# Kernel optimization log

Measured on AMD Instinct MI355X. Metric: run time of the kernel, lower is better.

## Reference

```python
import jax, jax.numpy as jnp
import numpy as np

C = 256
EPS = 1e-5


def dwconv3x3(x, w):
    # x: [B,C,H,W], w: [C,1,3,3] depthwise (groups=C)
    return jax.lax.conv_general_dilated(
        x, w, window_strides=(1, 1), padding=((1, 1), (1, 1)),
        dimension_numbers=('NCHW', 'OIHW', 'NCHW'), feature_group_count=x.shape[1])


def bn(x, gamma, beta, mean, var):
    # inference-mode batchnorm over channel dim of NCHW
    inv = gamma * jax.lax.rsqrt(var + EPS)
    return x * inv[:, None, None] + (beta - mean * inv)[:, None, None]


def setup_inputs() -> dict:
    key = jax.random.key(0)
    ks = jax.random.split(key, 8)
    B, H, W = 32, 64, 64
    inp = {
        'x': jax.random.normal(ks[0], (B, C, H, W), jnp.float32),
        'edge_w': jax.random.normal(ks[1], (C, 1, 3, 3), jnp.float32) * 0.1,
        'edge_gamma': jnp.ones((C,), jnp.float32),
        'edge_beta': jnp.zeros((C,), jnp.float32),
        'edge_mean': jnp.zeros((C,), jnp.float32),
        'edge_var': jnp.ones((C,), jnp.float32),
        'fc1_w': jax.random.normal(ks[2], (C // 16, C), jnp.float32) * 0.05,
        'fc2_w': jax.random.normal(ks[3], (C, C // 16), jnp.float32) * 0.05,
        'fusion_w': jax.random.normal(ks[4], (C, 2 * C), jnp.float32) * 0.05,
        'fusion_b': jnp.zeros((C,), jnp.float32),
        'bn1_gamma': jnp.ones((C,), jnp.float32),
        'bn1_beta': jnp.zeros((C,), jnp.float32),
        'bn1_mean': jnp.zeros((C,), jnp.float32),
        'bn1_var': jnp.ones((C,), jnp.float32),
        'deform_w': jax.random.normal(ks[5], (C, 1, 3, 3), jnp.float32) * 0.1,
        'balance_w': jax.random.normal(ks[6], (C, C), jnp.float32) * 0.05,
        'balance_b': jnp.zeros((C,), jnp.float32),
        'bn2_gamma': jnp.ones((C,), jnp.float32),
        'bn2_beta': jnp.zeros((C,), jnp.float32),
        'bn2_mean': jnp.zeros((C,), jnp.float32),
        'bn2_var': jnp.ones((C,), jnp.float32),
    }
    return inp


def reference(x, edge_w, edge_gamma, edge_beta, edge_mean, edge_var,
              fc1_w, fc2_w, fusion_w, fusion_b,
              bn1_gamma, bn1_beta, bn1_mean, bn1_var,
              deform_w, balance_w, balance_b,
              bn2_gamma, bn2_beta, bn2_mean, bn2_var):
    # --- EdgeEnhancementAttention ---
    edge = jax.nn.relu(bn(dwconv3x3(x, edge_w), edge_gamma, edge_beta, edge_mean, edge_var))
    # SE channel attention
    avg = jnp.mean(x, axis=(2, 3))                       # [B,C]
    att = jax.nn.relu(avg @ fc1_w.T)                     # [B,C/16]
    att = jax.nn.sigmoid(att @ fc2_w.T)                  # [B,C]
    enhanced = x * att[:, :, None, None]
    fused = jnp.concatenate([enhanced, edge], axis=1)    # [B,2C,H,W]
    out = jnp.einsum('bchw,oc->bohw', fused, fusion_w) + fusion_b[None, :, None, None]
    out = bn(out, bn1_gamma, bn1_beta, bn1_mean, bn1_var)
    # --- DeformConv2d with zero offsets == plain depthwise 3x3 conv, no bias ---
    out = dwconv3x3(out, deform_w)
    # --- balance: 1x1 conv + BN, then gate by input ---
    out = jnp.einsum('bchw,oc->bohw', out, balance_w) + balance_b[None, :, None, None]
    out = bn(out, bn2_gamma, bn2_beta, bn2_mean, bn2_var)
    return out * x
```

## Files before the change

kernel.cpp:

```cpp
#include <hip/hip_runtime.h>
#include <math.h>

#define HW 4096
#define PLSTRIDE ((size_t)HW * 8)

typedef unsigned short ushort_t;
typedef short v8s __attribute__((ext_vector_type(8)));
typedef float v4f __attribute__((ext_vector_type(4)));

__device__ __forceinline__ float bf2f(ushort_t u) {
    union { unsigned int i; float f; } v; v.i = ((unsigned int)u) << 16; return v.f;
}
__device__ __forceinline__ ushort_t f2bf(float f) {
    unsigned int x = __float_as_uint(f);
    x += 0x7fffu + ((x >> 16) & 1u);
    return (ushort_t)(x >> 16);
}

__device__ __forceinline__ void gld16(const ushort_t* g, ushort_t* l) {
    __builtin_amdgcn_global_load_lds(
        (__attribute__((address_space(1))) void*)g,
        (__attribute__((address_space(3))) void*)l, 16, 0, 0);
}

__global__ __launch_bounds__(256) void k_consts(
    const float* eg, const float* ebt, const float* em, const float* ev,
    const float* fb,
    const float* g1, const float* b1, const float* m1, const float* v1,
    const float* balb,
    const float* g2, const float* b2, const float* m2, const float* v2,
    float* cbuf)
{
    int c = threadIdx.x;
    float iE = eg[c] * rsqrtf(ev[c] + 1e-5f);
    cbuf[c]       = iE;
    cbuf[256 + c] = ebt[c] - em[c] * iE;
    float i1 = g1[c] * rsqrtf(v1[c] + 1e-5f);
    cbuf[512 + c] = i1;
    cbuf[768 + c] = b1[c] - m1[c] * i1 + fb[c] * i1;
    float i2 = g2[c] * rsqrtf(v2[c] + 1e-5f);
    cbuf[1024 + c] = i2;
    cbuf[1280 + c] = b2[c] - m2[c] * i2 + balb[c] * i2;
}

__global__ __launch_bounds__(256) void k_wcopy(const float* fusw, const float* balw,
                                               ushort_t* fusw2b, ushort_t* balwb)
{
    int o = blockIdx.x, t = threadIdx.x;
    fusw2b[o * 256 + t] = f2bf(fusw[o * 512 + 256 + t]);
    balwb[o * 256 + t]  = f2bf(balw[o * 256 + t]);
}

__global__ __launch_bounds__(512) void k_edge(const float* x, const float* ew,
                                              const float* cbuf, ushort_t* A,
                                              float* avg)
{
    __shared__ __align__(16) ushort_t Xs[4096];
    __shared__ __align__(16) ushort_t Es[4096];
    int cg = blockIdx.x;
    int b = blockIdx.y;
    int t = threadIdx.x;
    int w = t & 63;
    int pl = t >> 6;
    int c = cg * 8 + pl;
    const float* px = x + ((size_t)(b * 256 + c)) * HW;
    ushort_t* AX = A + ((size_t)(b * 64 + cg)) * PLSTRIDE;
    ushort_t* AE = A + ((size_t)(b * 64 + 32 + cg)) * PLSTRIDE;
    float wt[9];
    #pragma unroll
    for (int k = 0; k < 9; ++k) wt[k] = ew[c * 9 + k];
    float sE = cbuf[c], cE = cbuf[256 + c];
    bool wl = (w > 0), wrr = (w < 63);

    float p0l = 0.f, p0c = 0.f, p0r = 0.f;
    float p1l, p1c, p1r;
    p1c = px[w];
    p1l = wl ? px[w - 1] : 0.f;
    p1r = wrr ? px[w + 1] : 0.f;
    float s = 0.f;
    for (int hb = 0; hb < 8; ++hb) {
        #pragma unroll
        for (int hi = 0; hi < 8; ++hi) {
            int h = hb * 8 + hi;
            float p2l, p2c, p2r;
            if (h < 63) {
                const float* row = px + (h + 1) * 64;
                p2c = row[w];
                p2l = wl ? row[w - 1] : 0.f;
                p2r = wrr ? row[w + 1] : 0.f;
            } else {
                p2l = p2c = p2r = 0.f;
            }
            float a = p0l * wt[0] + p0c * wt[1] + p0r * wt[2]
                    + p1l * wt[3] + p1c * wt[4] + p1r * wt[5]
                    + p2l * wt[6] + p2c * wt[7] + p2r * wt[8];
            s += p1c;
            float v = a * sE + cE;
            Es[hi * 512 + w * 8 + pl] = f2bf(v > 0.f ? v : 0.f);
            Xs[hi * 512 + w * 8 + pl] = f2bf(p1c);
            p0l = p1l; p0c = p1c; p0r = p1r;
            p1l = p2l; p1c = p2c; p1r = p2r;
        }
        __syncthreads();
        {
            int hwg = (hb * 8 + pl) * 64 + w;
            uint4 vx = *(const uint4*)&Xs[pl * 512 + w * 8];
            uint4 ve = *(const uint4*)&Es[pl * 512 + w * 8];
            *(uint4*)(AX + (size_t)hwg * 8) = vx;
            *(uint4*)(AE + (size_t)hwg * 8) = ve;
        }
        __syncthreads();
    }
    #pragma unroll
    for (int off = 32; off > 0; off >>= 1) s += __shfl_down(s, off, 64);
    if ((t & 63) == 0) avg[b * 256 + c] = s * (1.0f / HW);
}

__global__ __launch_bounds__(256) void k_sefold(const float* avg, const float* fc1,
                                                const float* fc2, const float* fusw,
                                                ushort_t* w1b)
{
    int b = blockIdx.x, t = threadIdx.x;
    __shared__ float av[256];
    __shared__ float hid[16];
    av[t] = avg[b * 256 + t];
    __syncthreads();
    if (t < 16) {
        float h = 0.f;
        for (int c = 0; c < 256; ++c) h += av[c] * fc1[t * 256 + c];
        hid[t] = h > 0.f ? h : 0.f;
    }
    __syncthreads();
    float a = 0.f;
    #pragma unroll
    for (int j = 0; j < 16; ++j) a += hid[j] * fc2[t * 16 + j];
    float att = 1.0f / (1.0f + expf(-a));
    ushort_t* wout = w1b + (size_t)b * 65536;
    for (int o = 0; o < 256; ++o)
        wout[o * 256 + t] = f2bf(fusw[o * 512 + t] * att);
}

__global__ __launch_bounds__(512) void k_gemm1(ushort_t* __restrict__ A,
                                               const ushort_t* __restrict__ w1b,
                                               const ushort_t* __restrict__ fusw2b,
                                               const float* __restrict__ cbuf)
{
    __shared__ __align__(16) ushort_t At[8][64 * 64];
    int hw0 = blockIdx.x * 64;
    int b = blockIdx.y;
    int t = threadIdx.x;
    int lane = t & 63, wv = t >> 6;
    int quad = lane >> 4, l16 = lane & 15;
    int wr = wv >> 2, wc = wv & 3;

    int mrow0 = wv * 8 + (lane >> 3);
    int cswz = (lane & 7) ^ (mrow0 & 7);
    const ushort_t* srcK = A + ((size_t)(b * 64 + cswz)) * PLSTRIDE
                             + ((size_t)(hw0 + mrow0)) * 8;
    #pragma unroll
    for (int kb = 0; kb < 8; ++kb)
        gld16(srcK + (size_t)(kb * 8) * PLSTRIDE, &At[kb][wv * 8 * 64]);

    v4f acc[2][4];
    #pragma unroll
    for (int i = 0; i < 2; ++i)
        #pragma unroll
        for (int j = 0; j < 4; ++j) acc[i][j] = (v4f){0.f, 0.f, 0.f, 0.f};

    const ushort_t* rowA[4];
    const ushort_t* rowB[4];
    int oo[4];
    #pragma unroll
    for (int nt = 0; nt < 4; ++nt) {
        int o = wc * 64 + nt * 16 + l16;
        oo[nt] = o;
        rowA[nt] = w1b + ((size_t)(b * 256 + o)) * 256;
        rowB[nt] = fusw2b + (size_t)o * 256;
    }

#define LDB1(dst, kbv) { \
    _Pragma("unroll") for (int ks2 = 0; ks2 < 2; ++ks2) { \
        int kg = (kbv) * 64 + ks2 * 32 + quad * 8; \
        _Pragma("unroll") for (int nt = 0; nt < 4; ++nt) { \
            dst[ks2][nt] = ((kbv) < 4) ? *(const v8s*)(rowA[nt] + kg) \
                                       : *(const v8s*)(rowB[nt] + (kg - 256)); \
        } } }

#define COMP1(kbv, bsrc) { \
    _Pragma("unroll") for (int ks2 = 0; ks2 < 2; ++ks2) { \
        v8s afr[2]; \
        _Pragma("unroll") for (int mt = 0; mt < 2; ++mt) { \
            int ml = wr * 32 + mt * 16 + l16; \
            int jj = (ks2 * 4 + quad) ^ (ml & 7); \
            afr[mt] = *(const v8s*)(&At[kbv][ml * 64 + jj * 8]); \
        } \
        _Pragma("unroll") for (int mt = 0; mt < 2; ++mt) \
            _Pragma("unroll") for (int nt = 0; nt < 4; ++nt) \
                acc[mt][nt] = __builtin_amdgcn_mfma_f32_16x16x32_bf16( \
                    afr[mt], bsrc[ks2][nt], acc[mt][nt], 0, 0, 0); \
    } }

    v8s bq0[2][4], bq1[2][4];
    LDB1(bq0, 0);
    __syncthreads();
    #pragma unroll 1
    for (int kb = 0; kb < 8; kb += 2) {
        LDB1(bq1, kb + 1);
        COMP1(kb, bq0);
        if (kb < 6) LDB1(bq0, kb + 2);
        COMP1(kb + 1, bq1);
    }
#undef LDB1
#undef COMP1

    #pragma unroll
    for (int nt = 0; nt < 4; ++nt) {
        int o = oo[nt];
        float s1 = cbuf[512 + o], c1 = cbuf[768 + o];
        ushort_t* op = A + ((size_t)(b * 64 + 32 + (o >> 3))) * PLSTRIDE + (o & 7);
        #pragma unroll
        for (int mt = 0; mt < 2; ++mt)
            #pragma unroll
            for (int r = 0; r < 4; ++r) {
                int m = hw0 + wr * 32 + mt * 16 + quad * 4 + r;
                op[(size_t)m * 8] = f2bf(acc[mt][nt][r] * s1 + c1);
            }
    }
}

__global__ __launch_bounds__(256) void k_dw2(ushort_t* A, const float* dfw)
{
    int h = blockIdx.x;
    int b = blockIdx.y;
    int t = threadIdx.x;
    int wc = t & 7;
    int cg = t >> 3;
    int c0 = cg * 8;
    int w0 = wc * 8;

    float acc[8][8];
    #pragma unroll
    for (int w = 0; w < 8; ++w)
        #pragma unroll
        for (int ch = 0; ch < 8; ++ch) acc[w][ch] = 0.f;

    const ushort_t* pE = A + ((size_t)(b * 64 + 32 + cg)) * PLSTRIDE;
    #pragma unroll
    for (int r = 0; r < 3; ++r) {
        int hh = h - 1 + r;
        if (hh < 0 || hh > 63) continue;
        float wtr[3][8];
        #pragma unroll
        for (int d = 0; d < 3; ++d)
            #pragma unroll
            for (int ch = 0; ch < 8; ++ch)
                wtr[d][ch] = dfw[(c0 + ch) * 9 + r * 3 + d];
        const ushort_t* row = pE + (size_t)(hh * 64) * 8;
        uint4 rv[10];
        #pragma unroll
        for (int j = 0; j < 10; ++j) {
            int col = w0 - 1 + j;
            if (col >= 0 && col < 64)
                rv[j] = *(const uint4*)(row + (size_t)col * 8);
            else
                rv[j] = (uint4){0u, 0u, 0u, 0u};
        }
        #pragma unroll
        for (int j = 0; j < 10; ++j) {
            unsigned int wd[4] = { rv[j].x, rv[j].y, rv[j].z, rv[j].w };
            float v[8];
            #pragma unroll
            for (int i = 0; i < 8; ++i)
                v[i] = bf2f((i & 1) ? (ushort_t)(wd[i >> 1] >> 16)
                                    : (ushort_t)(wd[i >> 1] & 0xffff));
            if (j <= 7)
                #pragma unroll
                for (int ch = 0; ch < 8; ++ch) acc[j][ch] += v[ch] * wtr[0][ch];
            if (j >= 1 && j <= 8)
                #pragma unroll
                for (int ch = 0; ch < 8; ++ch) acc[j - 1][ch] += v[ch] * wtr[1][ch];
            if (j >= 2)
                #pragma unroll
                for (int ch = 0; ch < 8; ++ch) acc[j - 2][ch] += v[ch] * wtr[2][ch];
        }
    }
    ushort_t* pX = A + ((size_t)(b * 64 + cg)) * PLSTRIDE + (size_t)(h * 64 + w0) * 8;
    #pragma unroll
    for (int w = 0; w < 8; ++w) {
        uint4 ov;
        ov.x = (unsigned int)f2bf(acc[w][0]) | ((unsigned int)f2bf(acc[w][1]) << 16);
        ov.y = (unsigned int)f2bf(acc[w][2]) | ((unsigned int)f2bf(acc[w][3]) << 16);
        ov.z = (unsigned int)f2bf(acc[w][4]) | ((unsigned int)f2bf(acc[w][5]) << 16);
        ov.w = (unsigned int)f2bf(acc[w][6]) | ((unsigned int)f2bf(acc[w][7]) << 16);
        *(uint4*)(pX + (size_t)w * 8) = ov;
    }
}

__global__ __launch_bounds__(512) void k_gemm2(ushort_t* __restrict__ A,
                                               const ushort_t* __restrict__ balwb)
{
    __shared__ __align__(16) ushort_t At[4][128 * 64];
    int hw0 = blockIdx.x * 128;
    int b = blockIdx.y;
    int t = threadIdx.x;
    int lane = t & 63, wv = t >> 6;
    int quad = lane >> 4, l16 = lane & 15;
    int wr = wv >> 2, wc = wv & 3;

    int mrow0 = wv * 16 + (lane >> 3);
    int cswz = (lane & 7) ^ (mrow0 & 7);
    const ushort_t* srcK = A + ((size_t)(b * 64 + cswz)) * PLSTRIDE
                             + ((size_t)(hw0 + mrow0)) * 8;
    #pragma unroll
    for (int kb = 0; kb < 4; ++kb) {
        const ushort_t* sp = srcK + (size_t)(kb * 8) * PLSTRIDE;
        gld16(sp, &At[kb][(wv * 16) * 64]);
        gld16(sp + 64, &At[kb][(wv * 16 + 8) * 64]);
    }

    v4f acc[4][4];
    #pragma unroll
    for (int i = 0; i < 4; ++i)
        #pragma unroll
        for (int j = 0; j < 4; ++j) acc[i][j] = (v4f){0.f, 0.f, 0.f, 0.f};

    const ushort_t* rowW[4];
    int oo[4];
    #pragma unroll
    for (int nt = 0; nt < 4; ++nt) {
        int o = wc * 64 + nt * 16 + l16;
        oo[nt] = o;
        rowW[nt] = balwb + (size_t)o * 256;
    }

#define LDB2(dst, kbv) { \
    _Pragma("unroll") for (int ks2 = 0; ks2 < 2; ++ks2) { \
        int kg = (kbv) * 64 + ks2 * 32 + quad * 8; \
        _Pragma("unroll") for (int nt = 0; nt < 4; ++nt) \
            dst[ks2][nt] = *(const v8s*)(rowW[nt] + kg); \
    } }

#define COMP2(kbv, bsrc) { \
    _Pragma("unroll") for (int ks2 = 0; ks2 < 2; ++ks2) { \
        v8s afr[4]; \
        _Pragma("unroll") for (int mt = 0; mt < 4; ++mt) { \
            int ml = wr * 64 + mt * 16 + l16; \
            int jj = (ks2 * 4 + quad) ^ (ml & 7); \
            afr[mt] = *(const v8s*)(&At[kbv][ml * 64 + jj * 8]); \
        } \
        _Pragma("unroll") for (int mt = 0; mt < 4; ++mt) \
            _Pragma("unroll") for (int nt = 0; nt < 4; ++nt) \
                acc[mt][nt] = __builtin_amdgcn_mfma_f32_16x16x32_bf16( \
                    afr[mt], bsrc[ks2][nt], acc[mt][nt], 0, 0, 0); \
    } }

    v8s bq0[2][4], bq1[2][4];
    LDB2(bq0, 0);
    __syncthreads();
    #pragma unroll 1
    for (int kb = 0; kb < 4; kb += 2) {
        LDB2(bq1, kb + 1);
        COMP2(kb, bq0);
        if (kb < 2) LDB2(bq0, kb + 2);
        COMP2(kb + 1, bq1);
    }
#undef LDB2
#undef COMP2

    #pragma unroll
    for (int nt = 0; nt < 4; ++nt) {
        int o = oo[nt];
        ushort_t* op = A + ((size_t)(b * 64 + 32 + (o >> 3))) * PLSTRIDE + (o & 7);
        #pragma unroll
        for (int mt = 0; mt < 4; ++mt)
            #pragma unroll
            for (int r = 0; r < 4; ++r) {
                int m = hw0 + wr * 64 + mt * 16 + quad * 4 + r;
                op[(size_t)m * 8] = f2bf(acc[mt][nt][r]);
            }
    }
}

__global__ __launch_bounds__(256) void k_final(const ushort_t* A, const float* x,
                                               const float* cbuf, float* out)
{
    __shared__ float Lt[64 * 65];
    int bid = blockIdx.x;
    int b = bid >> 8;
    int rem = bid & 255;
    int hw0 = (rem >> 2) * 64;
    int c0 = (rem & 3) * 64;
    int t = threadIdx.x;
    #pragma unroll
    for (int r = 0; r < 2; ++r) {
        int idx = r * 256 + t;
        int hwl = idx >> 3;
        int cq = idx & 7;
        uint4 v = *(const uint4*)(A + ((size_t)(b * 64 + 32 + (c0 >> 3) + cq)) * PLSTRIDE
                                    + (size_t)(hw0 + hwl) * 8);
        unsigned int wd[4] = { v.x, v.y, v.z, v.w };
        #pragma unroll
        for (int j = 0; j < 8; ++j) {
            ushort_t u = (j & 1) ? (ushort_t)(wd[j >> 1] >> 16) : (ushort_t)(wd[j >> 1] & 0xffff);
            Lt[(cq * 8 + j) * 65 + hwl] = bf2f(u);
        }
    }
    __syncthreads();
    int hw_l = t & 63;
    int c_l0 = t >> 6;
    #pragma unroll
    for (int j = 0; j < 16; ++j) {
        int c_l = c_l0 * 16 + j;
        int c = c0 + c_l;
        float s2 = cbuf[1024 + c], c2 = cbuf[1280 + c];
        size_t g = ((size_t)b * 256 + c) * HW + hw0 + hw_l;
        float xv = x[g];
        out[g] = (Lt[c_l * 65 + hw_l] * s2 + c2) * xv;
    }
}

extern "C" void kernel_launch(void* const* d_in, const int* in_sizes, int n_in,
                              void* d_out, int out_size, void* d_ws, size_t ws_size,
                              hipStream_t stream)
{
    const float* x    = (const float*)d_in[0];
    const float* ew   = (const float*)d_in[1];
    const float* fc1  = (const float*)d_in[6];
    const float* fc2  = (const float*)d_in[7];
    const float* fusw = (const float*)d_in[8];
    const float* dfw  = (const float*)d_in[14];
    const float* balw = (const float*)d_in[15];
    float* out = (float*)d_out;

    char* ws = (char*)d_ws;
    ushort_t* A      = (ushort_t*)(ws);
    ushort_t* w1b    = (ushort_t*)(ws + 134217728);
    ushort_t* fusw2b = (ushort_t*)(ws + 138412032);
    ushort_t* balwb  = (ushort_t*)(ws + 138543104);
    float*    avg    = (float*)(ws + 138674176);
    float*    cbuf   = (float*)(ws + 138706944);

    k_consts<<<1, 256, 0, stream>>>((const float*)d_in[2], (const float*)d_in[3],
                                    (const float*)d_in[4], (const float*)d_in[5],
                                    (const float*)d_in[9],
                                    (const float*)d_in[10], (const float*)d_in[11],
                                    (const float*)d_in[12], (const float*)d_in[13],
                                    (const float*)d_in[16],
                                    (const float*)d_in[17], (const float*)d_in[18],
                                    (const float*)d_in[19], (const float*)d_in[20],
                                    cbuf);
    k_wcopy<<<256, 256, 0, stream>>>(fusw, balw, fusw2b, balwb);
    k_edge<<<dim3(32, 32), 512, 0, stream>>>(x, ew, cbuf, A, avg);
    k_sefold<<<32, 256, 0, stream>>>(avg, fc1, fc2, fusw, w1b);
    k_gemm1<<<dim3(64, 32), 512, 0, stream>>>(A, w1b, fusw2b, cbuf);
    k_dw2<<<dim3(64, 32), 256, 0, stream>>>(A, dfw);
    k_gemm2<<<dim3(32, 32), 512, 0, stream>>>(A, balwb);
    k_final<<<8192, 256, 0, stream>>>(A, x, cbuf, out);
}
```

Baseline: 648.5 us.

## Restructure GEMMs with LDS-staged B tiles, XCD swizzle, and sliding-row depthwise conv

Both 1x1-conv GEMMs now use 128x256 tiles that stage the A and B operands into LDS each K step through global_load_lds, replacing per-lane B register loads. A block-index remap spreads consecutive blocks across XCDs. The depthwise conv is rewritten so each thread owns one column and slides down 32 rows, reusing rows in registers and taking horizontal neighbours via lane shuffles. The final kernel's load indexing is reordered for coalescing. The GEMMs have no double buffering and sync twice per K step, which may expose load latency.

```diff
diff --git a/kernel.cpp b/kernel.cpp
--- a/kernel.cpp
+++ b/kernel.cpp
@@ -140,236 +140,220 @@
         wout[o * 256 + t] = f2bf(fusw[o * 512 + t] * att);
 }
 
-__global__ __launch_bounds__(512) void k_gemm1(ushort_t* __restrict__ A,
-                                               const ushort_t* __restrict__ w1b,
-                                               const ushort_t* __restrict__ fusw2b,
-                                               const float* __restrict__ cbuf)
-{
-    __shared__ __align__(16) ushort_t At[8][64 * 64];
-    int hw0 = blockIdx.x * 64;
-    int b = blockIdx.y;
+__global__ __launch_bounds__(512, 4) void k_gemm1(ushort_t* __restrict__ A,
+                                                  const ushort_t* __restrict__ w1b,
+                                                  const ushort_t* __restrict__ fusw2b,
+                                                  const float* __restrict__ cbuf)
+{
+    __shared__ __align__(16) ushort_t At[128 * 64];
+    __shared__ __align__(16) ushort_t Bt[256 * 64];
+    int bid = blockIdx.x;
+    int orig = (bid & 7) * 128 + (bid >> 3);
+    int b = orig >> 5;
+    int hw0 = (orig & 31) * 128;
     int t = threadIdx.x;
     int lane = t & 63, wv = t >> 6;
     int quad = lane >> 4, l16 = lane & 15;
     int wr = wv >> 2, wc = wv & 3;
-
-    int mrow0 = wv * 8 + (lane >> 3);
-    int cswz = (lane & 7) ^ (mrow0 & 7);
-    const ushort_t* srcK = A + ((size_t)(b * 64 + cswz)) * PLSTRIDE
-                             + ((size_t)(hw0 + mrow0)) * 8;
-    #pragma unroll
-    for (int kb = 0; kb < 8; ++kb)
-        gld16(srcK + (size_t)(kb * 8) * PLSTRIDE, &At[kb][wv * 8 * 64]);
-
-    v4f acc[2][4];
-    #pragma unroll
-    for (int i = 0; i < 2; ++i)
+    int srow = lane >> 3, kch = lane & 7;
+
+    v4f acc[4][4];
+    #pragma unroll
+    for (int i = 0; i < 4; ++i)
         #pragma unroll
         for (int j = 0; j < 4; ++j) acc[i][j] = (v4f){0.f, 0.f, 0.f, 0.f};
 
-    const ushort_t* rowA[4];
-    const ushort_t* rowB[4];
-    int oo[4];
+    for (int kb = 0; kb < 8; ++kb) {
+        __syncthreads();
+        #pragma unroll
+        for (int r = 0; r < 2; ++r) {
+            int mrow = wv * 8 + r * 64 + srow;
+            int csw = kch ^ (mrow & 7);
+            gld16(A + ((size_t)(b * 64 + kb * 8 + csw)) * PLSTRIDE
+                    + (size_t)(hw0 + mrow) * 8,
+                  &At[(wv * 8 + r * 64) * 64]);
+        }
+        #pragma unroll
+        for (int r = 0; r < 4; ++r) {
+            int orow = wv * 8 + r * 64 + srow;
+            int kc2 = kch ^ (orow & 7);
+            const ushort_t* bs = (kb < 4)
+                ? (w1b + ((size_t)(b * 256 + orow)) * 256 + kb * 64 + kc2 * 8)
+                : (fusw2b + ((size_t)orow) * 256 + (kb - 4) * 64 + kc2 * 8);
+            gld16(bs, &Bt[(wv * 8 + r * 64) * 64]);
+        }
+        __syncthreads();
+        #pragma unroll
+        for (int ks2 = 0; ks2 < 2; ++ks2) {
+            v8s afr[4], bfr[4];
+            #pragma unroll
+            for (int mt = 0; mt < 4; ++mt) {
+                int ml = wr * 64 + mt * 16 + l16;
+                int jj = (ks2 * 4 + quad) ^ (ml & 7);
+                afr[mt] = *(const v8s*)(&At[ml * 64 + jj * 8]);
+            }
+            #pragma unroll
+            for (int nt = 0; nt < 4; ++nt) {
+                int ol = wc * 64 + nt * 16 + l16;
+                int jj = (ks2 * 4 + quad) ^ (ol & 7);
+                bfr[nt] = *(const v8s*)(&Bt[ol * 64 + jj * 8]);
+            }
+            #pragma unroll
+            for (int mt = 0; mt < 4; ++mt)
+                #pragma unroll
+                for (int nt = 0; nt < 4; ++nt)
+                    acc[mt][nt] = __builtin_amdgcn_mfma_f32_16x16x32_bf16(
+                        afr[mt], bfr[nt], acc[mt][nt], 0, 0, 0);
+        }
+    }
+
     #pragma unroll
     for (int nt = 0; nt < 4; ++nt) {
         int o = wc * 64 + nt * 16 + l16;
-        oo[nt] = o;
-        rowA[nt] = w1b + ((size_t)(b * 256 + o)) * 256;
-        rowB[nt] = fusw2b + (size_t)o * 256;
-    }
-
-#define LDB1(dst, kbv) { \
-    _Pragma("unroll") for (int ks2 = 0; ks2 < 2; ++ks2) { \
-        int kg = (kbv) * 64 + ks2 * 32 + quad * 8; \
-        _Pragma("unroll") for (int nt = 0; nt < 4; ++nt) { \
-            dst[ks2][nt] = ((kbv) < 4) ? *(const v8s*)(rowA[nt] + kg) \
-                                       : *(const v8s*)(rowB[nt] + (kg - 256)); \
-        } } }
-
-#define COMP1(kbv, bsrc) { \
-    _Pragma("unroll") for (int ks2 = 0; ks2 < 2; ++ks2) { \
-        v8s afr[2]; \
-        _Pragma("unroll") for (int mt = 0; mt < 2; ++mt) { \
-            int ml = wr * 32 + mt * 16 + l16; \
-            int jj = (ks2 * 4 + quad) ^ (ml & 7); \
-            afr[mt] = *(const v8s*)(&At[kbv][ml * 64 + jj * 8]); \
-        } \
-        _Pragma("unroll") for (int mt = 0; mt < 2; ++mt) \
-            _Pragma("unroll") for (int nt = 0; nt < 4; ++nt) \
-                acc[mt][nt] = __builtin_amdgcn_mfma_f32_16x16x32_bf16( \
-                    afr[mt], bsrc[ks2][nt], acc[mt][nt], 0, 0, 0); \
-    } }
-
-    v8s bq0[2][4], bq1[2][4];
-    LDB1(bq0, 0);
-    __syncthreads();
-    #pragma unroll 1
-    for (int kb = 0; kb < 8; kb += 2) {
-        LDB1(bq1, kb + 1);
-        COMP1(kb, bq0);
-        if (kb < 6) LDB1(bq0, kb + 2);
-        COMP1(kb + 1, bq1);
-    }
-#undef LDB1
-#undef COMP1
-
-    #pragma unroll
-    for (int nt = 0; nt < 4; ++nt) {
-        int o = oo[nt];
         float s1 = cbuf[512 + o], c1 = cbuf[768 + o];
         ushort_t* op = A + ((size_t)(b * 64 + 32 + (o >> 3))) * PLSTRIDE + (o & 7);
         #pragma unroll
-        for (int mt = 0; mt < 2; ++mt)
+        for (int mt = 0; mt < 4; ++mt)
             #pragma unroll
             for (int r = 0; r < 4; ++r) {
-                int m = hw0 + wr * 32 + mt * 16 + quad * 4 + r;
+                int m = hw0 + wr * 64 + mt * 16 + quad * 4 + r;
                 op[(size_t)m * 8] = f2bf(acc[mt][nt][r] * s1 + c1);
             }
     }
 }
 
-__global__ __launch_bounds__(256) void k_dw2(ushort_t* A, const float* dfw)
-{
-    int h = blockIdx.x;
+__global__ __launch_bounds__(256) void k_dw2(ushort_t* __restrict__ A,
+                                             const float* __restrict__ dfw)
+{
+    int t = threadIdx.x;
+    int w = t & 63;
+    int pl = t >> 6;
+    int cg = blockIdx.x * 4 + pl;
     int b = blockIdx.y;
-    int t = threadIdx.x;
-    int wc = t & 7;
-    int cg = t >> 3;
-    int c0 = cg * 8;
-    int w0 = wc * 8;
-
-    float acc[8][8];
-    #pragma unroll
-    for (int w = 0; w < 8; ++w)
-        #pragma unroll
-        for (int ch = 0; ch < 8; ++ch) acc[w][ch] = 0.f;
-
+    int h0 = blockIdx.z * 32;
     const ushort_t* pE = A + ((size_t)(b * 64 + 32 + cg)) * PLSTRIDE;
-    #pragma unroll
-    for (int r = 0; r < 3; ++r) {
-        int hh = h - 1 + r;
-        if (hh < 0 || hh > 63) continue;
-        float wtr[3][8];
+    ushort_t* pX = A + ((size_t)(b * 64 + cg)) * PLSTRIDE;
+    float wt[3][3][8];
+    #pragma unroll
+    for (int r = 0; r < 3; ++r)
         #pragma unroll
         for (int d = 0; d < 3; ++d)
             #pragma unroll
             for (int ch = 0; ch < 8; ++ch)
-                wtr[d][ch] = dfw[(c0 + ch) * 9 + r * 3 + d];
-        const ushort_t* row = pE + (size_t)(hh * 64) * 8;
-        uint4 rv[10];
-        #pragma unroll
-        for (int j = 0; j < 10; ++j) {
-            int col = w0 - 1 + j;
-            if (col >= 0 && col < 64)
-                rv[j] = *(const uint4*)(row + (size_t)col * 8);
-            else
-                rv[j] = (uint4){0u, 0u, 0u, 0u};
-        }
-        #pragma unroll
-        for (int j = 0; j < 10; ++j) {
-            unsigned int wd[4] = { rv[j].x, rv[j].y, rv[j].z, rv[j].w };
-            float v[8];
-            #pragma unroll
-            for (int i = 0; i < 8; ++i)
-                v[i] = bf2f((i & 1) ? (ushort_t)(wd[i >> 1] >> 16)
-                                    : (ushort_t)(wd[i >> 1] & 0xffff));
-            if (j <= 7)
-                #pragma unroll
-                for (int ch = 0; ch < 8; ++ch) acc[j][ch] += v[ch] * wtr[0][ch];
-            if (j >= 1 && j <= 8)
-                #pragma unroll
-                for (int ch = 0; ch < 8; ++ch) acc[j - 1][ch] += v[ch] * wtr[1][ch];
-            if (j >= 2)
-                #pragma unroll
-                for (int ch = 0; ch < 8; ++ch) acc[j - 2][ch] += v[ch] * wtr[2][ch];
-        }
-    }
-    ushort_t* pX = A + ((size_t)(b * 64 + cg)) * PLSTRIDE + (size_t)(h * 64 + w0) * 8;
-    #pragma unroll
-    for (int w = 0; w < 8; ++w) {
+                wt[r][d][ch] = dfw[(cg * 8 + ch) * 9 + r * 3 + d];
+    bool wl = (w > 0), wrr = (w < 63);
+
+    uint4 rm, rc, rp;
+    rm = (h0 > 0) ? *(const uint4*)(pE + (size_t)((h0 - 1) * 64 + w) * 8)
+                  : (uint4){0u, 0u, 0u, 0u};
+    rc = *(const uint4*)(pE + (size_t)(h0 * 64 + w) * 8);
+
+#define DWROW(v, r) { \
+    unsigned int cx0 = v.x, cx1 = v.y, cx2 = v.z, cx3 = v.w; \
+    unsigned int lx0 = __shfl_up(cx0, 1, 64), lx1 = __shfl_up(cx1, 1, 64); \
+    unsigned int lx2 = __shfl_up(cx2, 1, 64), lx3 = __shfl_up(cx3, 1, 64); \
+    unsigned int rx0 = __shfl_down(cx0, 1, 64), rx1 = __shfl_down(cx1, 1, 64); \
+    unsigned int rx2 = __shfl_down(cx2, 1, 64), rx3 = __shfl_down(cx3, 1, 64); \
+    unsigned int cw[4] = { cx0, cx1, cx2, cx3 }; \
+    unsigned int lw[4] = { lx0, lx1, lx2, lx3 }; \
+    unsigned int rw[4] = { rx0, rx1, rx2, rx3 }; \
+    _Pragma("unroll") for (int ch = 0; ch < 8; ++ch) { \
+        float fC = bf2f((ch & 1) ? (ushort_t)(cw[ch >> 1] >> 16) \
+                                 : (ushort_t)(cw[ch >> 1] & 0xffff)); \
+        float fL = wl ? bf2f((ch & 1) ? (ushort_t)(lw[ch >> 1] >> 16) \
+                                      : (ushort_t)(lw[ch >> 1] & 0xffff)) : 0.f; \
+        float fR = wrr ? bf2f((ch & 1) ? (ushort_t)(rw[ch >> 1] >> 16) \
+                                       : (ushort_t)(rw[ch >> 1] & 0xffff)) : 0.f; \
+        acc[ch] += fL * wt[r][0][ch] + fC * wt[r][1][ch] + fR * wt[r][2][ch]; \
+    } }
+
+    for (int s = 0; s < 32; ++s) {
+        int h = h0 + s;
+        rp = (h + 1 < 64) ? *(const uint4*)(pE + (size_t)((h + 1) * 64 + w) * 8)
+                          : (uint4){0u, 0u, 0u, 0u};
+        float acc[8];
+        #pragma unroll
+        for (int ch = 0; ch < 8; ++ch) acc[ch] = 0.f;
+        DWROW(rm, 0);
+        DWROW(rc, 1);
+        DWROW(rp, 2);
         uint4 ov;
-        ov.x = (unsigned int)f2bf(acc[w][0]) | ((unsigned int)f2bf(acc[w][1]) << 16);
-        ov.y = (unsigned int)f2bf(acc[w][2]) | ((unsigned int)f2bf(acc[w][3]) << 16);
-        ov.z = (unsigned int)f2bf(acc[w][4]) | ((unsigned int)f2bf(acc[w][5]) << 16);
-        ov.w = (unsigned int)f2bf(acc[w][6]) | ((unsigned int)f2bf(acc[w][7]) << 16);
-        *(uint4*)(pX + (size_t)w * 8) = ov;
-    }
-}
-
-__global__ __launch_bounds__(512) void k_gemm2(ushort_t* __restrict__ A,
-                                               const ushort_t* __restrict__ balwb)
-{
-    __shared__ __align__(16) ushort_t At[4][128 * 64];
-    int hw0 = blockIdx.x * 128;
-    int b = blockIdx.y;
+        ov.x = (unsigned int)f2bf(acc[0]) | ((unsigned int)f2bf(acc[1]) << 16);
+        ov.y = (unsigned int)f2bf(acc[2]) | ((unsigned int)f2bf(acc[3]) << 16);
+        ov.z = (unsigned int)f2bf(acc[4]) | ((unsigned int)f2bf(acc[5]) << 16);
+        ov.w = (unsigned int)f2bf(acc[6]) | ((unsigned int)f2bf(acc[7]) << 16);
+        *(uint4*)(pX + (size_t)(h * 64 + w) * 8) = ov;
+        rm = rc; rc = rp;
+    }
+#undef DWROW
+}
+
+__global__ __launch_bounds__(512, 4) void k_gemm2(ushort_t* __restrict__ A,
+                                                  const ushort_t* __restrict__ balwb)
+{
+    __shared__ __align__(16) ushort_t At[128 * 64];
+    __shared__ __align__(16) ushort_t Bt[256 * 64];
+    int bid = blockIdx.x;
+    int orig = (bid & 7) * 128 + (bid >> 3);
+    int b = orig >> 5;
+    int hw0 = (orig & 31) * 128;
     int t = threadIdx.x;
     int lane = t & 63, wv = t >> 6;
     int quad = lane >> 4, l16 = lane & 15;
     int wr = wv >> 2, wc = wv & 3;
-
-    int mrow0 = wv * 16 + (lane >> 3);
-    int cswz = (lane & 7) ^ (mrow0 & 7);
-    const ushort_t* srcK = A + ((size_t)(b * 64 + cswz)) * PLSTRIDE
-                             + ((size_t)(hw0 + mrow0)) * 8;
-    #pragma unroll
+    int srow = lane >> 3, kch = lane & 7;
+
+    v4f acc[4][4];
+    #pragma unroll
+    for (int i = 0; i < 4; ++i)
+        #pragma unroll
+        for (int j = 0; j < 4; ++j) acc[i][j] = (v4f){0.f, 0.f, 0.f, 0.f};
+
     for (int kb = 0; kb < 4; ++kb) {
-        const ushort_t* sp = srcK + (size_t)(kb * 8) * PLSTRIDE;
-        gld16(sp, &At[kb][(wv * 16) * 64]);
-        gld16(sp + 64, &At[kb][(wv * 16 + 8) * 64]);
-    }
-
-    v4f acc[4][4];
-    #pragma unroll
-    for (int i = 0; i < 4; ++i)
-        #pragma unroll
-        for (int j = 0; j < 4; ++j) acc[i][j] = (v4f){0.f, 0.f, 0.f, 0.f};
-
-    const ushort_t* rowW[4];
-    int oo[4];
+        __syncthreads();
+        #pragma unroll
+        for (int r = 0; r < 2; ++r) {
+            int mrow = wv * 8 + r * 64 + srow;
+            int csw = kch ^ (mrow & 7);
+            gld16(A + ((size_t)(b * 64 + kb * 8 + csw)) * PLSTRIDE
+                    + (size_t)(hw0 + mrow) * 8,
+                  &At[(wv * 8 + r * 64) * 64]);
+        }
+        #pragma unroll
+        for (int r = 0; r < 4; ++r) {
+            int orow = wv * 8 + r * 64 + srow;
+            int kc2 = kch ^ (orow & 7);
+            gld16(balwb + ((size_t)orow) * 256 + kb * 64 + kc2 * 8,
+                  &Bt[(wv * 8 + r * 64) * 64]);
+        }
+        __syncthreads();
+        #pragma unroll
+        for (int ks2 = 0; ks2 < 2; ++ks2) {
+            v8s afr[4], bfr[4];
+            #pragma unroll
+            for (int mt = 0; mt < 4; ++mt) {
+                int ml = wr * 64 + mt * 16 + l16;
+                int jj = (ks2 * 4 + quad) ^ (ml & 7);
+                afr[mt] = *(const v8s*)(&At[ml * 64 + jj * 8]);
+            }
+            #pragma unroll
+            for (int nt = 0; nt < 4; ++nt) {
+                int ol = wc * 64 + nt * 16 + l16;
+                int jj = (ks2 * 4 + quad) ^ (ol & 7);
+                bfr[nt] = *(const v8s*)(&Bt[ol * 64 + jj * 8]);
+            }
+            #pragma unroll
+            for (int mt = 0; mt < 4; ++mt)
+                #pragma unroll
+                for (int nt = 0; nt < 4; ++nt)
+                    acc[mt][nt] = __builtin_amdgcn_mfma_f32_16x16x32_bf16(
+                        afr[mt], bfr[nt], acc[mt][nt], 0, 0, 0);
+        }
+    }
+
     #pragma unroll
     for (int nt = 0; nt < 4; ++nt) {
         int o = wc * 64 + nt * 16 + l16;
-        oo[nt] = o;
-        rowW[nt] = balwb + (size_t)o * 256;
-    }
-
-#define LDB2(dst, kbv) { \
-    _Pragma("unroll") for (int ks2 = 0; ks2 < 2; ++ks2) { \
-        int kg = (kbv) * 64 + ks2 * 32 + quad * 8; \
-        _Pragma("unroll") for (int nt = 0; nt < 4; ++nt) \
-            dst[ks2][nt] = *(const v8s*)(rowW[nt] + kg); \
-    } }
-
-#define COMP2(kbv, bsrc) { \
-    _Pragma("unroll") for (int ks2 = 0; ks2 < 2; ++ks2) { \
-        v8s afr[4]; \
-        _Pragma("unroll") for (int mt = 0; mt < 4; ++mt) { \
-            int ml = wr * 64 + mt * 16 + l16; \
-            int jj = (ks2 * 4 + quad) ^ (ml & 7); \
-            afr[mt] = *(const v8s*)(&At[kbv][ml * 64 + jj * 8]); \
-        } \
-        _Pragma("unroll") for (int mt = 0; mt < 4; ++mt) \
-            _Pragma("unroll") for (int nt = 0; nt < 4; ++nt) \
-                acc[mt][nt] = __builtin_amdgcn_mfma_f32_16x16x32_bf16( \
-                    afr[mt], bsrc[ks2][nt], acc[mt][nt], 0, 0, 0); \
-    } }
-
-    v8s bq0[2][4], bq1[2][4];
-    LDB2(bq0, 0);
-    __syncthreads();
-    #pragma unroll 1
-    for (int kb = 0; kb < 4; kb += 2) {
-        LDB2(bq1, kb + 1);
-        COMP2(kb, bq0);
-        if (kb < 2) LDB2(bq0, kb + 2);
-        COMP2(kb + 1, bq1);
-    }
-#undef LDB2
-#undef COMP2
-
-    #pragma unroll
-    for (int nt = 0; nt < 4; ++nt) {
-        int o = oo[nt];
         ushort_t* op = A + ((size_t)(b * 64 + 32 + (o >> 3))) * PLSTRIDE + (o & 7);
         #pragma unroll
         for (int mt = 0; mt < 4; ++mt)
@@ -394,8 +378,8 @@
     #pragma unroll
     for (int r = 0; r < 2; ++r) {
         int idx = r * 256 + t;
-        int hwl = idx >> 3;
-        int cq = idx & 7;
+        int cq = idx >> 6;
+        int hwl = idx & 63;
         uint4 v = *(const uint4*)(A + ((size_t)(b * 64 + 32 + (c0 >> 3) + cq)) * PLSTRIDE
                                     + (size_t)(hw0 + hwl) * 8);
         unsigned int wd[4] = { v.x, v.y, v.z, v.w };
@@ -452,8 +436,8 @@
     k_wcopy<<<256, 256, 0, stream>>>(fusw, balw, fusw2b, balwb);
     k_edge<<<dim3(32, 32), 512, 0, stream>>>(x, ew, cbuf, A, avg);
     k_sefold<<<32, 256, 0, stream>>>(avg, fc1, fc2, fusw, w1b);
-    k_gemm1<<<dim3(64, 32), 512, 0, stream>>>(A, w1b, fusw2b, cbuf);
-    k_dw2<<<dim3(64, 32), 256, 0, stream>>>(A, dfw);
-    k_gemm2<<<dim3(32, 32), 512, 0, stream>>>(A, balwb);
+    k_gemm1<<<1024, 512, 0, stream>>>(A, w1b, fusw2b, cbuf);
+    k_dw2<<<dim3(8, 32, 2), 256, 0, stream>>>(A, dfw);
+    k_gemm2<<<1024, 512, 0, stream>>>(A, balwb);
     k_final<<<8192, 256, 0, stream>>>(A, x, cbuf, out);
 }
```

After: 538.5 us. 1.2x faster.
